# Performance work log

Measured on AMD Instinct MI355X. Metric: run time of the kernel, lower is better.

## Reference

```python
import jax, jax.numpy as jnp
import numpy as np
import math

# Static multi-level spatial layout (H, W) per level and flattened start offsets.
SHAPES = ((100, 100), (50, 50), (25, 25), (13, 13))
STARTS = (0, 10000, 12500, 13125)
LEN_IN = 13294
D_MODEL, N_LEVELS, N_HEADS, N_POINTS = 256, 4, 8, 4
D_HEAD = D_MODEL // N_HEADS
B, LQ = 2, 13294


def _offset_bias():
    # Replicates MSDeformAttn._reset_parameters radial grid init for sampling_offsets.bias
    thetas = np.arange(N_HEADS, dtype=np.float32) * (2.0 * math.pi / N_HEADS)
    grid = np.stack([np.cos(thetas), np.sin(thetas)], axis=-1)  # [nh, 2]
    grid = grid / np.abs(grid).max(axis=-1, keepdims=True)
    # [nh, nl, np, 2] with per-point radius (i+1)
    full = np.tile(grid[:, None, None, :], (1, N_LEVELS, N_POINTS, 1))
    full = full * np.arange(1, N_POINTS + 1, dtype=np.float32)[None, None, :, None]
    return full.reshape(-1)


def setup_inputs() -> dict:
    key = jax.random.key(0)
    ks = jax.random.split(key, 8)
    xavier = 1.0 / math.sqrt(D_MODEL)
    return {
        "query": jax.random.normal(ks[0], (B, LQ, D_MODEL), jnp.float32),
        "reference_points": jax.random.uniform(ks[1], (B, LQ, N_LEVELS, 2), jnp.float32),
        "input_flatten": jax.random.normal(ks[2], (B, LEN_IN, D_MODEL), jnp.float32),
        "input_spatial_shapes": jnp.array(SHAPES, jnp.int32),
        "input_level_start_index": jnp.array(STARTS, jnp.int32),
        "W_off": jax.random.normal(ks[3], (D_MODEL, N_HEADS * N_LEVELS * N_POINTS * 2), jnp.float32) * 0.01,
        "b_off": jnp.asarray(_offset_bias()),
        "W_attn": jax.random.normal(ks[4], (D_MODEL, N_HEADS * N_LEVELS * N_POINTS), jnp.float32) * 0.02,
        "b_attn": jnp.zeros((N_HEADS * N_LEVELS * N_POINTS,), jnp.float32),
        "W_val": jax.random.normal(ks[5], (D_MODEL, D_MODEL), jnp.float32) * xavier,
        "b_val": jnp.zeros((D_MODEL,), jnp.float32),
        "W_out": jax.random.normal(ks[6], (D_MODEL, D_MODEL), jnp.float32) * xavier,
        "b_out": jnp.zeros((D_MODEL,), jnp.float32),
    }


def reference(query, reference_points, input_flatten, input_spatial_shapes,
              input_level_start_index, W_off, b_off, W_attn, b_attn,
              W_val, b_val, W_out, b_out):
    Bq, Lq, _ = query.shape
    value = (input_flatten @ W_val + b_val).reshape(Bq, LEN_IN, N_HEADS, D_HEAD)

    off = (query @ W_off + b_off).reshape(Bq, Lq, N_HEADS, N_LEVELS, N_POINTS, 2)
    aw = (query @ W_attn + b_attn).reshape(Bq, Lq, N_HEADS, N_LEVELS * N_POINTS)
    aw = jax.nn.softmax(aw, axis=-1).reshape(Bq, Lq, N_HEADS, N_LEVELS, N_POINTS)

    # offset normalizer is (W, H) per level
    normalizer = jnp.array([[w, h] for (h, w) in SHAPES], query.dtype)  # [nl, 2]
    loc = reference_points[:, :, None, :, None, :] + off / normalizer[None, None, None, :, None, :]

    bi = jnp.arange(Bq)[:, None, None, None]
    hi = jnp.arange(N_HEADS)[None, None, :, None]
    out = jnp.zeros((Bq, Lq, N_HEADS, D_HEAD), query.dtype)

    # Per-level zero-padded bilinear sampling (math-equivalent to grid_sample
    # align_corners=False, padding_mode='zeros' on the padded max_H x max_W grid,
    # since the padded region is zero-filled).
    for lvl, (H, W) in enumerate(SHAPES):
        s = STARTS[lvl]
        vflat = value[:, s:s + H * W]  # [B, H*W, nh, dh]
        l = loc[:, :, :, lvl]          # [B, Lq, nh, P, 2] in normalized coords
        x = l[..., 0] * W - 0.5
        y = l[..., 1] * H - 0.5
        x0 = jnp.floor(x)
        y0 = jnp.floor(y)
        sampled = jnp.zeros((Bq, Lq, N_HEADS, N_POINTS, D_HEAD), query.dtype)
        for dx in (0, 1):
            for dy in (0, 1):
                xi = x0 + dx
                yi = y0 + dy
                wgt = (1.0 - jnp.abs(x - xi)) * (1.0 - jnp.abs(y - yi))
                valid = (xi >= 0) & (xi <= W - 1) & (yi >= 0) & (yi <= H - 1)
                idx = (jnp.clip(yi, 0, H - 1) * W + jnp.clip(xi, 0, W - 1)).astype(jnp.int32)
                v = vflat[bi, idx, hi]  # [B, Lq, nh, P, dh]
                sampled = sampled + v * (wgt * valid)[..., None]
        out = out + jnp.einsum('bqhpd,bqhp->bqhd', sampled, aw[:, :, :, lvl])

    out = out.reshape(Bq, Lq, D_MODEL)
    return out @ W_out + b_out
```

## Files before the change

kernel.cpp:

```cpp
#include <hip/hip_runtime.h>
#include <math.h>

#define BQ 2
#define LQ 13294
#define LEN_IN 13294
#define M_ROWS 26588

__device__ __constant__ int c_HW[4]    = {100, 50, 25, 13};
__device__ __constant__ int c_START[4] = {0, 10000, 12500, 13125};

typedef __attribute__((ext_vector_type(8))) short bf16x8;
typedef __attribute__((ext_vector_type(4))) float f32x4;

__device__ inline unsigned short f2bf(float f) {
  union { float f; unsigned int u; } x; x.f = f;
  unsigned int u = x.u;
  return (unsigned short)((u + 0x7fffu + ((u >> 16) & 1u)) >> 16);
}
__device__ inline float h2f(unsigned short h) {
  _Float16 x; __builtin_memcpy(&x, &h, 2); return (float)x;
}
__device__ inline unsigned short f2h(float f) {
  _Float16 x = (_Float16)f; unsigned short u; __builtin_memcpy(&u, &x, 2); return u;
}

__device__ inline void gl_lds16(const void* g, void* l) {
  __builtin_amdgcn_global_load_lds(
      (const __attribute__((address_space(1))) unsigned int*)g,
      (__attribute__((address_space(3))) unsigned int*)l, 16, 0, 0);
}

#define CONV_BLKS 3456
#define N4EACH (M_ROWS * 64)

__global__ __launch_bounds__(256) void prep_all(
    const float* __restrict__ query, const float* __restrict__ inpf,
    const float* __restrict__ W_off, const float* __restrict__ b_off,
    const float* __restrict__ W_attn, const float* __restrict__ b_attn,
    const float* __restrict__ W_val, const float* __restrict__ W_out,
    unsigned short* __restrict__ q_bf, unsigned short* __restrict__ in_bf,
    unsigned short* __restrict__ Wval_t, unsigned short* __restrict__ Woa_t,
    unsigned short* __restrict__ Wout_t, float* __restrict__ b_oa) {
  const int bx = blockIdx.x;
  if (bx < CONV_BLKS) {
    int i = bx * 256 + threadIdx.x;
    const int stride = CONV_BLKS * 256;
    for (; i < 2 * N4EACH; i += stride) {
      const float* src; unsigned short* dst; int j;
      if (i < N4EACH) { src = query; dst = q_bf; j = i; }
      else            { src = inpf;  dst = in_bf; j = i - N4EACH; }
      const float4 v = ((const float4*)src)[j];
      ushort4 h;
      h.x = f2bf(v.x); h.y = f2bf(v.y); h.z = f2bf(v.z); h.w = f2bf(v.w);
      ((ushort4*)dst)[j] = h;
    }
    return;
  }
  const int idx = (bx - CONV_BLKS) * 256 + threadIdx.x;
  const int SZ1 = 256 * 256;
  const int SZ2 = 384 * 256;
  if (idx < SZ1) {
    const int n = idx >> 8, k = idx & 255;
    Wval_t[idx] = f2bf(W_val[k * 256 + n]);
  } else if (idx < SZ1 + SZ2) {
    const int j = idx - SZ1;
    const int n = j >> 8, k = j & 255;
    const float v = (n < 256) ? W_off[k * 256 + n] : W_attn[k * 128 + (n - 256)];
    Woa_t[j] = f2bf(v);
  } else {
    const int j = idx - SZ1 - SZ2;
    const int n = j >> 8, k = j & 255;
    Wout_t[j] = f2bf(W_out[k * 256 + n]);
  }
  if (bx == CONV_BLKS) b_oa[threadIdx.x] = b_off[threadIdx.x];
  if (bx == CONV_BLKS + 1 && threadIdx.x < 128)
    b_oa[256 + threadIdx.x] = b_attn[threadIdx.x];
}

template <int CT>
__device__ inline void gemm_stream(
    const unsigned short* __restrict__ A, const unsigned short* __restrict__ Wt,
    const float* __restrict__ bias, void* __restrict__ Cp,
    int M, int N, int m0, int n0, unsigned short* Ws) {
  const int tid = threadIdx.x;
  const int wv = tid >> 6;
  const int lane = tid & 63;
  const int fr = lane & 15;
  const int fq = lane >> 4;

#pragma unroll
  for (int it = 0; it < 16; ++it) {
    const int lin = wv * 1024 + it * 64 + lane;
    const int r = lin >> 5;
    const int p = lin & 31;
    const int c = p ^ (r & 7);
    gl_lds16(Wt + (size_t)(n0 + r) * 256 + c * 8,
             &Ws[(size_t)(wv * 1024 + it * 64) * 8]);
  }
  __syncthreads();

  int mr0 = m0 + wv * 32 + fr;       if (mr0 > M - 1) mr0 = M - 1;
  int mr1 = m0 + wv * 32 + 16 + fr;  if (mr1 > M - 1) mr1 = M - 1;
  const unsigned short* a0 = A + (size_t)mr0 * 256 + fq * 8;
  const unsigned short* a1 = A + (size_t)mr1 * 256 + fq * 8;

  f32x4 acc[2][8];
#pragma unroll
  for (int mt = 0; mt < 2; ++mt)
#pragma unroll
    for (int n = 0; n < 8; ++n) acc[mt][n] = (f32x4){0.f, 0.f, 0.f, 0.f};

#pragma unroll
  for (int kk = 0; kk < 8; ++kk) {
    const bf16x8 af0 = *(const bf16x8*)(a0 + kk * 32);
    const bf16x8 af1 = *(const bf16x8*)(a1 + kk * 32);
#pragma unroll
    for (int n = 0; n < 8; ++n) {
      const int rn = n * 16 + fr;
      const bf16x8 b =
          *(const bf16x8*)&Ws[rn * 256 + (((kk * 4 + fq) ^ (rn & 7)) * 8)];
      acc[0][n] = __builtin_amdgcn_mfma_f32_16x16x32_bf16(b, af0, acc[0][n], 0, 0, 0);
      acc[1][n] = __builtin_amdgcn_mfma_f32_16x16x32_bf16(b, af1, acc[1][n], 0, 0, 0);
    }
  }

#pragma unroll
  for (int n = 0; n < 8; ++n) {
    const int nb = n0 + n * 16 + fq * 4;
    const float4 b4 = *(const float4*)&bias[nb];
#pragma unroll
    for (int mt = 0; mt < 2; ++mt) {
      const int m = m0 + wv * 32 + mt * 16 + fr;
      if (m >= M) continue;
      const float v0 = acc[mt][n][0] + b4.x;
      const float v1 = acc[mt][n][1] + b4.y;
      const float v2 = acc[mt][n][2] + b4.z;
      const float v3 = acc[mt][n][3] + b4.w;
      if (CT == 0) {
        *(float4*)&((float*)Cp)[(size_t)m * N + nb] = make_float4(v0, v1, v2, v3);
      } else if (CT == 1) {
        uint2 o;
        o.x = (unsigned int)f2bf(v0) | ((unsigned int)f2bf(v1) << 16);
        o.y = (unsigned int)f2bf(v2) | ((unsigned int)f2bf(v3) << 16);
        *(uint2*)&((unsigned short*)Cp)[(size_t)m * N + nb] = o;
      } else {
        uint2 o;
        o.x = (unsigned int)f2h(v0) | ((unsigned int)f2h(v1) << 16);
        o.y = (unsigned int)f2h(v2) | ((unsigned int)f2h(v3) << 16);
        *(uint2*)&((unsigned short*)Cp)[(size_t)m * N + nb] = o;
      }
    }
  }
}

__global__ __launch_bounds__(256) void gemm_vo(
    const unsigned short* __restrict__ in_bf,
    const unsigned short* __restrict__ q_bf,
    const unsigned short* __restrict__ Wval_t,
    const unsigned short* __restrict__ Woa_t,
    const float* __restrict__ b_val, const float* __restrict__ b_oa,
    void* __restrict__ v_buf, void* __restrict__ oa_buf) {
  __shared__ unsigned short Ws[128 * 256];
  const int m0 = blockIdx.x * 128;
  if (blockIdx.y < 2) {
    gemm_stream<1>(in_bf, Wval_t, b_val, v_buf, M_ROWS, 256,
                   m0, blockIdx.y * 128, Ws);
  } else {
    gemm_stream<2>(q_bf, Woa_t, b_oa, oa_buf, M_ROWS, 384,
                   m0, (blockIdx.y - 2) * 128, Ws);
  }
}

__global__ __launch_bounds__(256) void gemm_out(
    const unsigned short* __restrict__ mid,
    const unsigned short* __restrict__ Wout_t,
    const float* __restrict__ b_out, float* __restrict__ out) {
  __shared__ unsigned short Ws[128 * 256];
  gemm_stream<0>(mid, Wout_t, b_out, out, M_ROWS, 256,
                 blockIdx.x * 128, blockIdx.y * 128, Ws);
}

__global__ __launch_bounds__(256) void sample_kernel(
    const float* __restrict__ refp,
    const unsigned short* __restrict__ oa,
    const unsigned short* __restrict__ value,
    unsigned int* __restrict__ mid) {
  const int tid = threadIdx.x;
  const int qi = tid >> 7;
  const int q = blockIdx.x * 2 + qi;
  const int b = (q >= LQ) ? 1 : 0;

  __shared__ float2 s_wo[2][4][136];

  {
    const int pid = tid & 127;
    const int h = pid >> 4;
    const int lp = pid & 15;
    const int l = lp >> 2;
    const int p = lp & 3;
    const int HW = c_HW[l];
    const float fW = (float)HW;

    const float logit = h2f(oa[(size_t)q * 384 + 256 + pid]);
    float mx = logit;
#pragma unroll
    for (int s = 1; s < 16; s <<= 1) mx = fmaxf(mx, __shfl_xor(mx, s, 16));
    const float e = expf(logit - mx);
    float sum = e;
#pragma unroll
    for (int s = 1; s < 16; s <<= 1) sum += __shfl_xor(sum, s, 16);
    const float a = e / sum;

    const unsigned int opk =
        *(const unsigned int*)&oa[(size_t)q * 384 + h * 32 + l * 8 + p * 2];
    const float ox = h2f((unsigned short)(opk & 0xffffu));
    const float oy = h2f((unsigned short)(opk >> 16));
    const float rx = refp[((size_t)q * 4 + l) * 2 + 0];
    const float ry = refp[((size_t)q * 4 + l) * 2 + 1];
    const float x = (rx + ox / fW) * fW - 0.5f;
    const float y = (ry + oy / fW) * fW - 0.5f;
    const float x0 = floorf(x);
    const float y0 = floorf(y);

#pragma unroll
    for (int t = 0; t < 4; ++t) {
      const int dx = t & 1;
      const int dy = t >> 1;
      const float xi = x0 + (float)dx;
      const float yi = y0 + (float)dy;
      const float wgt = (1.0f - fabsf(x - xi)) * (1.0f - fabsf(y - yi));
      const bool valid =
          (xi >= 0.f) && (xi <= fW - 1.f) && (yi >= 0.f) && (yi <= fW - 1.f);
      int xc = (int)xi; xc = xc < 0 ? 0 : (xc > HW - 1 ? HW - 1 : xc);
      int yc = (int)yi; yc = yc < 0 ? 0 : (yc > HW - 1 ? HW - 1 : yc);
      const int row = b * LEN_IN + c_START[l] + yc * HW + xc;
      float2 wo;
      wo.x = valid ? wgt * a : 0.f;
      wo.y = __int_as_float(row * 512 + h * 64);
      s_wo[qi][t][h * 17 + lp] = wo;
    }
  }
  __syncthreads();

  {
    const int g = tid & 127;
    const int h = g >> 4;
    const int dp = g & 15;
    const char* vbase = (const char*)value + dp * 4;
    float acc0 = 0.f, acc1 = 0.f;
#pragma unroll 4
    for (int lp = 0; lp < 16; ++lp) {
      const int si = h * 17 + lp;
#pragma unroll
      for (int t = 0; t < 4; ++t) {
        const float2 f = s_wo[qi][t][si];
        const unsigned int v = *(const unsigned int*)(vbase + __float_as_int(f.y));
        acc0 += f.x * __uint_as_float(v << 16);
        acc1 += f.x * __uint_as_float(v & 0xffff0000u);
      }
    }
    mid[(size_t)q * 128 + h * 16 + dp] =
        (unsigned int)f2bf(acc0) | ((unsigned int)f2bf(acc1) << 16);
  }
}

extern "C" void kernel_launch(void* const* d_in, const int* in_sizes, int n_in,
                              void* d_out, int out_size, void* d_ws,
                              size_t ws_size, hipStream_t stream) {
  const float* query  = (const float*)d_in[0];
  const float* refp   = (const float*)d_in[1];
  const float* inpf   = (const float*)d_in[2];
  const float* W_off  = (const float*)d_in[5];
  const float* b_off  = (const float*)d_in[6];
  const float* W_attn = (const float*)d_in[7];
  const float* b_attn = (const float*)d_in[8];
  const float* W_val  = (const float*)d_in[9];
  const float* b_val  = (const float*)d_in[10];
  const float* W_out  = (const float*)d_in[11];
  const float* b_out  = (const float*)d_in[12];
  float* out = (float*)d_out;

  unsigned char* w = (unsigned char*)d_ws;
  unsigned short* Wval_t = (unsigned short*)w;  w += 256 * 256 * 2;
  unsigned short* Woa_t  = (unsigned short*)w;  w += 384 * 256 * 2;
  unsigned short* Wout_t = (unsigned short*)w;  w += 256 * 256 * 2;
  float*          b_oa   = (float*)w;           w += 384 * 4 + 64;
  unsigned short* q_bf   = (unsigned short*)w;  w += (size_t)M_ROWS * 256 * 2;
  unsigned short* in_bf  = (unsigned short*)w;  w += (size_t)M_ROWS * 256 * 2;
  unsigned short* v_buf  = (unsigned short*)w;  w += (size_t)M_ROWS * 256 * 2;
  unsigned short* oa_buf = (unsigned short*)w;  w += (size_t)M_ROWS * 384 * 2;
  unsigned int*   mid_buf = (unsigned int*)w;

  const dim3 blk(256);
  const int mg = (M_ROWS + 127) / 128;

  prep_all<<<dim3(CONV_BLKS + 896), blk, 0, stream>>>(
      query, inpf, W_off, b_off, W_attn, b_attn, W_val, W_out,
      q_bf, in_bf, Wval_t, Woa_t, Wout_t, b_oa);
  gemm_vo<<<dim3(mg, 5), blk, 0, stream>>>(in_bf, q_bf, Wval_t, Woa_t,
                                           b_val, b_oa, v_buf, oa_buf);
  sample_kernel<<<dim3(M_ROWS / 2), blk, 0, stream>>>(refp, oa_buf, v_buf,
                                                      mid_buf);
  gemm_out<<<dim3(mg, 2), blk, 0, stream>>>((const unsigned short*)mid_buf,
                                            Wout_t, b_out, out);
}
```

Before: 212.6 us.

## Fuse fp32-to-bf16 activation conversion into GEMM A-operand loads

```diff
diff --git a/kernel.cpp b/kernel.cpp
--- a/kernel.cpp
+++ b/kernel.cpp
@@ -11,6 +11,7 @@
 
 typedef __attribute__((ext_vector_type(8))) short bf16x8;
 typedef __attribute__((ext_vector_type(4))) float f32x4;
+typedef __attribute__((ext_vector_type(2))) float f32x2;
 
 __device__ inline unsigned short f2bf(float f) {
   union { float f; unsigned int u; } x; x.f = f;
@@ -30,33 +31,13 @@
       (__attribute__((address_space(3))) unsigned int*)l, 16, 0, 0);
 }
 
-#define CONV_BLKS 3456
-#define N4EACH (M_ROWS * 64)
-
-__global__ __launch_bounds__(256) void prep_all(
-    const float* __restrict__ query, const float* __restrict__ inpf,
+__global__ __launch_bounds__(256) void prep_w(
     const float* __restrict__ W_off, const float* __restrict__ b_off,
     const float* __restrict__ W_attn, const float* __restrict__ b_attn,
     const float* __restrict__ W_val, const float* __restrict__ W_out,
-    unsigned short* __restrict__ q_bf, unsigned short* __restrict__ in_bf,
     unsigned short* __restrict__ Wval_t, unsigned short* __restrict__ Woa_t,
     unsigned short* __restrict__ Wout_t, float* __restrict__ b_oa) {
-  const int bx = blockIdx.x;
-  if (bx < CONV_BLKS) {
-    int i = bx * 256 + threadIdx.x;
-    const int stride = CONV_BLKS * 256;
-    for (; i < 2 * N4EACH; i += stride) {
-      const float* src; unsigned short* dst; int j;
-      if (i < N4EACH) { src = query; dst = q_bf; j = i; }
-      else            { src = inpf;  dst = in_bf; j = i - N4EACH; }
-      const float4 v = ((const float4*)src)[j];
-      ushort4 h;
-      h.x = f2bf(v.x); h.y = f2bf(v.y); h.z = f2bf(v.z); h.w = f2bf(v.w);
-      ((ushort4*)dst)[j] = h;
-    }
-    return;
-  }
-  const int idx = (bx - CONV_BLKS) * 256 + threadIdx.x;
+  const int idx = blockIdx.x * 256 + threadIdx.x;
   const int SZ1 = 256 * 256;
   const int SZ2 = 384 * 256;
   if (idx < SZ1) {
@@ -72,22 +53,13 @@
     const int n = j >> 8, k = j & 255;
     Wout_t[j] = f2bf(W_out[k * 256 + n]);
   }
-  if (bx == CONV_BLKS) b_oa[threadIdx.x] = b_off[threadIdx.x];
-  if (bx == CONV_BLKS + 1 && threadIdx.x < 128)
+  if (blockIdx.x == 0) b_oa[threadIdx.x] = b_off[threadIdx.x];
+  if (blockIdx.x == 1 && threadIdx.x < 128)
     b_oa[256 + threadIdx.x] = b_attn[threadIdx.x];
 }
 
-template <int CT>
-__device__ inline void gemm_stream(
-    const unsigned short* __restrict__ A, const unsigned short* __restrict__ Wt,
-    const float* __restrict__ bias, void* __restrict__ Cp,
-    int M, int N, int m0, int n0, unsigned short* Ws) {
-  const int tid = threadIdx.x;
-  const int wv = tid >> 6;
-  const int lane = tid & 63;
-  const int fr = lane & 15;
-  const int fq = lane >> 4;
-
+__device__ inline void stage_W(const unsigned short* __restrict__ Wt,
+                               int n0, int wv, int lane, unsigned short* Ws) {
 #pragma unroll
   for (int it = 0; it < 16; ++it) {
     const int lin = wv * 1024 + it * 64 + lane;
@@ -97,13 +69,13 @@
     gl_lds16(Wt + (size_t)(n0 + r) * 256 + c * 8,
              &Ws[(size_t)(wv * 1024 + it * 64) * 8]);
   }
-  __syncthreads();
-
-  int mr0 = m0 + wv * 32 + fr;       if (mr0 > M - 1) mr0 = M - 1;
-  int mr1 = m0 + wv * 32 + 16 + fr;  if (mr1 > M - 1) mr1 = M - 1;
-  const unsigned short* a0 = A + (size_t)mr0 * 256 + fq * 8;
-  const unsigned short* a1 = A + (size_t)mr1 * 256 + fq * 8;
-
+}
+
+template <int CT>
+__device__ inline void kloop_epilogue(
+    const bf16x8* a0f, const bf16x8* a1f, const unsigned short* Ws,
+    const float* __restrict__ bias, void* __restrict__ Cp,
+    int M, int N, int m0, int n0, int wv, int fr, int fq) {
   f32x4 acc[2][8];
 #pragma unroll
   for (int mt = 0; mt < 2; ++mt)
@@ -112,15 +84,13 @@
 
 #pragma unroll
   for (int kk = 0; kk < 8; ++kk) {
-    const bf16x8 af0 = *(const bf16x8*)(a0 + kk * 32);
-    const bf16x8 af1 = *(const bf16x8*)(a1 + kk * 32);
 #pragma unroll
     for (int n = 0; n < 8; ++n) {
       const int rn = n * 16 + fr;
       const bf16x8 b =
           *(const bf16x8*)&Ws[rn * 256 + (((kk * 4 + fq) ^ (rn & 7)) * 8)];
-      acc[0][n] = __builtin_amdgcn_mfma_f32_16x16x32_bf16(b, af0, acc[0][n], 0, 0, 0);
-      acc[1][n] = __builtin_amdgcn_mfma_f32_16x16x32_bf16(b, af1, acc[1][n], 0, 0, 0);
+      acc[0][n] = __builtin_amdgcn_mfma_f32_16x16x32_bf16(b, a0f[kk], acc[0][n], 0, 0, 0);
+      acc[1][n] = __builtin_amdgcn_mfma_f32_16x16x32_bf16(b, a1f[kk], acc[1][n], 0, 0, 0);
     }
   }
 
@@ -153,9 +123,76 @@
   }
 }
 
+template <int CT>
+__device__ inline void gemm_stream_f32A(
+    const float* __restrict__ A, const unsigned short* __restrict__ Wt,
+    const float* __restrict__ bias, void* __restrict__ Cp,
+    int M, int N, int m0, int n0, unsigned short* Ws) {
+  const int tid = threadIdx.x;
+  const int wv = tid >> 6;
+  const int lane = tid & 63;
+  const int fr = lane & 15;
+  const int fq = lane >> 4;
+
+  int mr0 = m0 + wv * 32 + fr;       if (mr0 > M - 1) mr0 = M - 1;
+  int mr1 = m0 + wv * 32 + 16 + fr;  if (mr1 > M - 1) mr1 = M - 1;
+  const float* a0 = A + (size_t)mr0 * 256 + fq * 8;
+  const float* a1 = A + (size_t)mr1 * 256 + fq * 8;
+
+  bf16x8 a0f[8], a1f[8];
+#pragma unroll
+  for (int kk = 0; kk < 8; ++kk) {
+    const float4 x0 = *(const float4*)(a0 + kk * 32);
+    const float4 x1 = *(const float4*)(a0 + kk * 32 + 4);
+    const float4 y0 = *(const float4*)(a1 + kk * 32);
+    const float4 y1 = *(const float4*)(a1 + kk * 32 + 4);
+    ushort4 h0, h1;
+    h0.x = f2bf(x0.x); h0.y = f2bf(x0.y); h0.z = f2bf(x0.z); h0.w = f2bf(x0.w);
+    h1.x = f2bf(x1.x); h1.y = f2bf(x1.y); h1.z = f2bf(x1.z); h1.w = f2bf(x1.w);
+    union { ushort4 h[2]; bf16x8 v; } u0; u0.h[0] = h0; u0.h[1] = h1;
+    a0f[kk] = u0.v;
+    h0.x = f2bf(y0.x); h0.y = f2bf(y0.y); h0.z = f2bf(y0.z); h0.w = f2bf(y0.w);
+    h1.x = f2bf(y1.x); h1.y = f2bf(y1.y); h1.z = f2bf(y1.z); h1.w = f2bf(y1.w);
+    union { ushort4 h[2]; bf16x8 v; } u1; u1.h[0] = h0; u1.h[1] = h1;
+    a1f[kk] = u1.v;
+  }
+
+  stage_W(Wt, n0, wv, lane, Ws);
+  __syncthreads();
+
+  kloop_epilogue<CT>(a0f, a1f, Ws, bias, Cp, M, N, m0, n0, wv, fr, fq);
+}
+
+template <int CT>
+__device__ inline void gemm_stream_bf16A(
+    const unsigned short* __restrict__ A, const unsigned short* __restrict__ Wt,
+    const float* __restrict__ bias, void* __restrict__ Cp,
+    int M, int N, int m0, int n0, unsigned short* Ws) {
+  const int tid = threadIdx.x;
+  const int wv = tid >> 6;
+  const int lane = tid & 63;
+  const int fr = lane & 15;
+  const int fq = lane >> 4;
+
+  int mr0 = m0 + wv * 32 + fr;       if (mr0 > M - 1) mr0 = M - 1;
+  int mr1 = m0 + wv * 32 + 16 + fr;  if (mr1 > M - 1) mr1 = M - 1;
+  const unsigned short* a0 = A + (size_t)mr0 * 256 + fq * 8;
+  const unsigned short* a1 = A + (size_t)mr1 * 256 + fq * 8;
+  bf16x8 a0f[8], a1f[8];
+#pragma unroll
+  for (int kk = 0; kk < 8; ++kk) {
+    a0f[kk] = *(const bf16x8*)(a0 + kk * 32);
+    a1f[kk] = *(const bf16x8*)(a1 + kk * 32);
+  }
+
+  stage_W(Wt, n0, wv, lane, Ws);
+  __syncthreads();
+
+  kloop_epilogue<CT>(a0f, a1f, Ws, bias, Cp, M, N, m0, n0, wv, fr, fq);
+}
+
 __global__ __launch_bounds__(256) void gemm_vo(
-    const unsigned short* __restrict__ in_bf,
-    const unsigned short* __restrict__ q_bf,
+    const float* __restrict__ inpf, const float* __restrict__ query,
     const unsigned short* __restrict__ Wval_t,
     const unsigned short* __restrict__ Woa_t,
     const float* __restrict__ b_val, const float* __restrict__ b_oa,
@@ -163,11 +200,11 @@
   __shared__ unsigned short Ws[128 * 256];
   const int m0 = blockIdx.x * 128;
   if (blockIdx.y < 2) {
-    gemm_stream<1>(in_bf, Wval_t, b_val, v_buf, M_ROWS, 256,
-                   m0, blockIdx.y * 128, Ws);
+    gemm_stream_f32A<1>(inpf, Wval_t, b_val, v_buf, M_ROWS, 256,
+                        m0, blockIdx.y * 128, Ws);
   } else {
-    gemm_stream<2>(q_bf, Woa_t, b_oa, oa_buf, M_ROWS, 384,
-                   m0, (blockIdx.y - 2) * 128, Ws);
+    gemm_stream_f32A<2>(query, Woa_t, b_oa, oa_buf, M_ROWS, 384,
+                        m0, (blockIdx.y - 2) * 128, Ws);
   }
 }
 
@@ -176,8 +213,8 @@
     const unsigned short* __restrict__ Wout_t,
     const float* __restrict__ b_out, float* __restrict__ out) {
   __shared__ unsigned short Ws[128 * 256];
-  gemm_stream<0>(mid, Wout_t, b_out, out, M_ROWS, 256,
-                 blockIdx.x * 128, blockIdx.y * 128, Ws);
+  gemm_stream_bf16A<0>(mid, Wout_t, b_out, out, M_ROWS, 256,
+                       blockIdx.x * 128, blockIdx.y * 128, Ws);
 }
 
 __global__ __launch_bounds__(256) void sample_kernel(
@@ -217,8 +254,8 @@
     const float oy = h2f((unsigned short)(opk >> 16));
     const float rx = refp[((size_t)q * 4 + l) * 2 + 0];
     const float ry = refp[((size_t)q * 4 + l) * 2 + 1];
-    const float x = (rx + ox / fW) * fW - 0.5f;
-    const float y = (ry + oy / fW) * fW - 0.5f;
+    const float x = fmaf(rx, fW, ox - 0.5f);
+    const float y = fmaf(ry, fW, oy - 0.5f);
     const float x0 = floorf(x);
     const float y0 = floorf(y);
 
@@ -247,7 +284,7 @@
     const int h = g >> 4;
     const int dp = g & 15;
     const char* vbase = (const char*)value + dp * 4;
-    float acc0 = 0.f, acc1 = 0.f;
+    f32x2 acc = {0.f, 0.f};
 #pragma unroll 4
     for (int lp = 0; lp < 16; ++lp) {
       const int si = h * 17 + lp;
@@ -255,12 +292,12 @@
       for (int t = 0; t < 4; ++t) {
         const float2 f = s_wo[qi][t][si];
         const unsigned int v = *(const unsigned int*)(vbase + __float_as_int(f.y));
-        acc0 += f.x * __uint_as_float(v << 16);
-        acc1 += f.x * __uint_as_float(v & 0xffff0000u);
+        f32x2 av = {__uint_as_float(v << 16), __uint_as_float(v & 0xffff0000u)};
+        acc += f.x * av;
       }
     }
     mid[(size_t)q * 128 + h * 16 + dp] =
-        (unsigned int)f2bf(acc0) | ((unsigned int)f2bf(acc1) << 16);
+        (unsigned int)f2bf(acc.x) | ((unsigned int)f2bf(acc.y) << 16);
   }
 }
 
@@ -285,8 +322,6 @@
   unsigned short* Woa_t  = (unsigned short*)w;  w += 384 * 256 * 2;
   unsigned short* Wout_t = (unsigned short*)w;  w += 256 * 256 * 2;
   float*          b_oa   = (float*)w;           w += 384 * 4 + 64;
-  unsigned short* q_bf   = (unsigned short*)w;  w += (size_t)M_ROWS * 256 * 2;
-  unsigned short* in_bf  = (unsigned short*)w;  w += (size_t)M_ROWS * 256 * 2;
   unsigned short* v_buf  = (unsigned short*)w;  w += (size_t)M_ROWS * 256 * 2;
   unsigned short* oa_buf = (unsigned short*)w;  w += (size_t)M_ROWS * 384 * 2;
   unsigned int*   mid_buf = (unsigned int*)w;
@@ -294,10 +329,10 @@
   const dim3 blk(256);
   const int mg = (M_ROWS + 127) / 128;
 
-  prep_all<<<dim3(CONV_BLKS + 896), blk, 0, stream>>>(
-      query, inpf, W_off, b_off, W_attn, b_attn, W_val, W_out,
-      q_bf, in_bf, Wval_t, Woa_t, Wout_t, b_oa);
-  gemm_vo<<<dim3(mg, 5), blk, 0, stream>>>(in_bf, q_bf, Wval_t, Woa_t,
+  prep_w<<<dim3(896), blk, 0, stream>>>(W_off, b_off, W_attn, b_attn,
+                                        W_val, W_out, Wval_t, Woa_t,
+                                        Wout_t, b_oa);
+  gemm_vo<<<dim3(mg, 5), blk, 0, stream>>>(inpf, query, Wval_t, Woa_t,
                                            b_val, b_oa, v_buf, oa_buf);
   sample_kernel<<<dim3(M_ROWS / 2), blk, 0, stream>>>(refp, oa_buf, v_buf,
                                                       mid_buf);
```

After: 209.8 us. Within noise of the previous version (-1.3%).
